# Optimization experiments

Hardware: AMD Instinct MI355X
Metric: run time of the kernel (lower is better)

Reference implementation:

```python
import jax, jax.numpy as jnp
import numpy as np

B, H, T, D = 4, 16, 2048, 128

def setup_inputs() -> dict:
    key = jax.random.key(0)
    kq, kk, kv = jax.random.split(key, 3)
    q = jax.random.normal(kq, (B, H, T, D), dtype=jnp.float32)
    k = jax.random.normal(kk, (B, H, T, D), dtype=jnp.float32)
    v = jax.random.normal(kv, (B, H, T, D), dtype=jnp.float32)
    return {"q": q, "k": k, "v": v}

def reference(q, k, v):
    # scores: [B,H,T,T] = q @ k^T, masked multiplicatively by causal lower-tri ones
    T_ = q.shape[-2]
    mask = jnp.tril(jnp.ones((T_, T_), dtype=q.dtype))  # CausalMulMask
    scores = jnp.einsum('bhid,bhjd->bhij', q, k) * mask
    # no softmax: linear attention, scores @ v
    return jnp.einsum('bhij,bhjd->bhid', scores, v)
```

## Files before the change

kernel.cpp:

```cpp
#include <hip/hip_runtime.h>
#include <stdint.h>

#define SEQ    2048
#define DIM    128
#define CHUNK  128
#define NCHUNK 16
#define NBH    64
#define DSLA   4
#define DCA    32

typedef __attribute__((ext_vector_type(8))) short short8;
typedef __attribute__((ext_vector_type(4))) float floatx4;

#define MFMA(a, b, c) __builtin_amdgcn_mfma_f32_16x16x32_bf16((a), (b), (c), 0, 0, 0)

__device__ __forceinline__ short f2bf(float f) {
  union { float f; uint32_t u; } x; x.f = f;
  uint32_t r = x.u + 0x7fffu + ((x.u >> 16) & 1u);
  return (short)(r >> 16);
}
__device__ __forceinline__ short8 pack8(const float4 a, const float4 b) {
  short8 s;
  s[0] = f2bf(a.x); s[1] = f2bf(a.y); s[2] = f2bf(a.z); s[3] = f2bf(a.w);
  s[4] = f2bf(b.x); s[5] = f2bf(b.y); s[6] = f2bf(b.z); s[7] = f2bf(b.w);
  return s;
}

__global__ __launch_bounds__(512, 2) void k_state(
    const float* __restrict__ kin, const float* __restrict__ vin,
    short* __restrict__ ws) {
  const int blk = blockIdx.x;
  const int bh  = blk & 63;
  const int dsl = blk >> 6;
  const int ds0 = dsl * DCA;
  const float* kb = kin + (size_t)bh * SEQ * DIM;
  const float* vb = vin + (size_t)bh * SEQ * DIM;

  __shared__ short Kt[128][136];
  __shared__ short Vt[DCA][136];
  __shared__ short Ss[DCA][136];

  const int tid  = threadIdx.x;
  const int wave = tid >> 6;
  const int lane = tid & 63;
  const int q4   = lane >> 4;
  const int l16  = lane & 15;
  const int j    = tid & 127;
  const int dhi  = tid >> 7;

  floatx4 acc[2];
#pragma unroll
  for (int mt = 0; mt < 2; ++mt)
#pragma unroll
    for (int r = 0; r < 4; ++r) acc[mt][r] = 0.f;

  float4 kreg[4][2], vreg[2];
  auto load_c = [&](int c) {
    const float* krow = kb + (size_t)(c * CHUNK + j) * DIM + dhi * 8;
#pragma unroll
    for (int it = 0; it < 4; ++it) {
      kreg[it][0] = *(const float4*)(krow + it * 32);
      kreg[it][1] = *(const float4*)(krow + it * 32 + 4);
    }
    const float* vrow = vb + (size_t)(c * CHUNK + j) * DIM + ds0 + dhi * 8;
    vreg[0] = *(const float4*)(vrow);
    vreg[1] = *(const float4*)(vrow + 4);
  };
  load_c(0);

  for (int c = 0; c < NCHUNK; ++c) {
    __syncthreads();

#pragma unroll
    for (int it = 0; it < 4; ++it) {
      const int d0 = it * 32 + dhi * 8;
      Kt[d0 + 0][j] = f2bf(kreg[it][0].x);
      Kt[d0 + 1][j] = f2bf(kreg[it][0].y);
      Kt[d0 + 2][j] = f2bf(kreg[it][0].z);
      Kt[d0 + 3][j] = f2bf(kreg[it][0].w);
      Kt[d0 + 4][j] = f2bf(kreg[it][1].x);
      Kt[d0 + 5][j] = f2bf(kreg[it][1].y);
      Kt[d0 + 6][j] = f2bf(kreg[it][1].z);
      Kt[d0 + 7][j] = f2bf(kreg[it][1].w);
    }
    {
      const int d0 = dhi * 8;
      Vt[d0 + 0][j] = f2bf(vreg[0].x);
      Vt[d0 + 1][j] = f2bf(vreg[0].y);
      Vt[d0 + 2][j] = f2bf(vreg[0].z);
      Vt[d0 + 3][j] = f2bf(vreg[0].w);
      Vt[d0 + 4][j] = f2bf(vreg[1].x);
      Vt[d0 + 5][j] = f2bf(vreg[1].y);
      Vt[d0 + 6][j] = f2bf(vreg[1].z);
      Vt[d0 + 7][j] = f2bf(vreg[1].w);
    }
#pragma unroll
    for (int mt = 0; mt < 2; ++mt)
#pragma unroll
      for (int r = 0; r < 4; ++r)
        Ss[mt * 16 + q4 * 4 + r][wave * 16 + l16] = f2bf(acc[mt][r]);

    __syncthreads();

    if (c + 1 < NCHUNK) load_c(c + 1);

    {
      const int ks2 = tid >> 7, tnl = (tid >> 6) & 1;
      const int q42 = (tid >> 4) & 3, l162 = tid & 15;
      const short8 sv = *(const short8*)&Ss[tnl * 16 + l162][ks2 * 32 + q42 * 8];
      *(short8*)&ws[((size_t)((bh * 16 + c) * 4 + dsl)) * 4096 + (size_t)tid * 8] = sv;
    }

#pragma unroll
    for (int ks = 0; ks < 4; ++ks) {
      const short8 bk = *(const short8*)&Kt[wave * 16 + l16][ks * 32 + q4 * 8];
#pragma unroll
      for (int mt = 0; mt < 2; ++mt) {
        const short8 av = *(const short8*)&Vt[mt * 16 + l16][ks * 32 + q4 * 8];
        acc[mt] = MFMA(av, bk, acc[mt]);
      }
    }
  }
}

__global__ __launch_bounds__(512, 2) void k_out(
    const float* __restrict__ qin, const float* __restrict__ kin,
    const float* __restrict__ vin, const short* __restrict__ ws,
    float* __restrict__ out) {
  const int blk = blockIdx.x;
  const int bh  = blk & 63;
  const int c   = blk >> 6;
  const size_t base = (size_t)bh * SEQ * DIM + (size_t)c * CHUNK * DIM;
  const float* qc = qin + base;
  const float* kc = kin + base;
  const float* vc = vin + base;
  float* oc = out + base;

  __shared__ short Klds[128][136];
  __shared__ short Vt[128][136];
  __shared__ short Ps[128][136];
  __shared__ short Sb[16384];

  const int tid  = threadIdx.x;
  const int wave = tid >> 6;
  const int lane = tid & 63;
  const int q4   = lane >> 4;
  const int l16  = lane & 15;
  const int j    = tid & 127;
  const int dhi  = tid >> 7;

  const float* qrow = qc + (size_t)(wave * 16 + l16) * DIM + q4 * 8;
  short8 aq[4];
#pragma unroll
  for (int ks = 0; ks < 4; ++ks)
    aq[ks] = pack8(*(const float4*)(qrow + ks * 32),
                   *(const float4*)(qrow + ks * 32 + 4));

#pragma unroll
  for (int it = 0; it < 4; ++it) {
    const int e = it * 4096 + tid * 8;
    *(short8*)&Klds[e >> 7][e & 127] =
        pack8(*(const float4*)(kc + e), *(const float4*)(kc + e + 4));
  }
#pragma unroll
  for (int it = 0; it < 4; ++it) {
    const int d0 = it * 32 + dhi * 8;
    const float* vrow = vc + (size_t)j * DIM + d0;
    const float4 a = *(const float4*)vrow;
    const float4 b = *(const float4*)(vrow + 4);
    Vt[d0 + 0][j] = f2bf(a.x); Vt[d0 + 1][j] = f2bf(a.y);
    Vt[d0 + 2][j] = f2bf(a.z); Vt[d0 + 3][j] = f2bf(a.w);
    Vt[d0 + 4][j] = f2bf(b.x); Vt[d0 + 5][j] = f2bf(b.y);
    Vt[d0 + 6][j] = f2bf(b.z); Vt[d0 + 7][j] = f2bf(b.w);
  }
  if (c > 0) {
    const short* sp = ws + (size_t)(bh * 16 + c) * 16384;
#pragma unroll
    for (int it = 0; it < 4; ++it) {
      const int off = it * 4096 + tid * 8;
      *(short8*)&Sb[off] = *(const short8*)&sp[off];
    }
  }
  __syncthreads();

  floatx4 oacc[8];
#pragma unroll
  for (int tn = 0; tn < 8; ++tn)
#pragma unroll
    for (int r = 0; r < 4; ++r) oacc[tn][r] = 0.f;

  if (c > 0) {
#pragma unroll
    for (int ks = 0; ks < 4; ++ks)
#pragma unroll
      for (int tn = 0; tn < 8; ++tn) {
        const short8 bs = *(const short8*)
            &Sb[(tn >> 1) * 4096 + ks * 1024 + (tn & 1) * 512 + lane * 8];
        oacc[tn] = MFMA(aq[ks], bs, oacc[tn]);
      }
  }

  for (int tj = 0; tj <= wave; ++tj) {
    floatx4 sacc;
#pragma unroll
    for (int r = 0; r < 4; ++r) sacc[r] = 0.f;
#pragma unroll
    for (int ks = 0; ks < 4; ++ks) {
      const short8 bk = *(const short8*)&Klds[tj * 16 + l16][ks * 32 + q4 * 8];
      sacc = MFMA(aq[ks], bk, sacc);
    }
#pragma unroll
    for (int r = 0; r < 4; ++r) {
      float val = sacc[r];
      if (tj == wave && l16 > q4 * 4 + r) val = 0.f;
      Ps[wave * 16 + q4 * 4 + r][tj * 16 + l16] = f2bf(val);
    }
  }
  if ((wave & 1) == 0) {
#pragma unroll
    for (int r = 0; r < 4; ++r)
      Ps[wave * 16 + q4 * 4 + r][(wave + 1) * 16 + l16] = 0;
  }

  const int kst = (wave + 2) >> 1;
  for (int t = 0; t < kst; ++t) {
    const short8 ap = *(const short8*)&Ps[wave * 16 + l16][t * 32 + q4 * 8];
#pragma unroll
    for (int tn = 0; tn < 8; ++tn) {
      const short8 bv = *(const short8*)&Vt[tn * 16 + l16][t * 32 + q4 * 8];
      oacc[tn] = MFMA(ap, bv, oacc[tn]);
    }
  }

#pragma unroll
  for (int tn = 0; tn < 8; ++tn)
#pragma unroll
    for (int r = 0; r < 4; ++r)
      oc[(size_t)(wave * 16 + q4 * 4 + r) * DIM + tn * 16 + l16] = oacc[tn][r];
}

extern "C" void kernel_launch(void* const* d_in, const int* in_sizes, int n_in,
                              void* d_out, int out_size, void* d_ws, size_t ws_size,
                              hipStream_t stream) {
  const float* q = (const float*)d_in[0];
  const float* k = (const float*)d_in[1];
  const float* v = (const float*)d_in[2];
  float* out = (float*)d_out;
  (void)in_sizes; (void)n_in; (void)out_size; (void)ws_size;
  short* ws = (short*)d_ws;

  hipLaunchKernelGGL(k_state, dim3(NBH * DSLA), dim3(512), 0, stream, k, v, ws);
  hipLaunchKernelGGL(k_out, dim3(NBH * NCHUNK), dim3(512), 0, stream,
                     q, k, v, ws, out);
}
```

Baseline: 285.0 us.

## Stage state-kernel loads via async LDS DMA and shrink output-kernel LDS

```diff
diff --git a/kernel.cpp b/kernel.cpp
--- a/kernel.cpp
+++ b/kernel.cpp
@@ -24,6 +24,11 @@
   s[0] = f2bf(a.x); s[1] = f2bf(a.y); s[2] = f2bf(a.z); s[3] = f2bf(a.w);
   s[4] = f2bf(b.x); s[5] = f2bf(b.y); s[6] = f2bf(b.z); s[7] = f2bf(b.w);
   return s;
+}
+__device__ __forceinline__ void gload16(const float* g, float* l) {
+  __builtin_amdgcn_global_load_lds(
+      (const __attribute__((address_space(1))) void*)g,
+      (__attribute__((address_space(3))) void*)l, 16, 0, 0);
 }
 
 __global__ __launch_bounds__(512, 2) void k_state(
@@ -36,6 +41,8 @@
   const float* kb = kin + (size_t)bh * SEQ * DIM;
   const float* vb = vin + (size_t)bh * SEQ * DIM;
 
+  __shared__ __align__(16) float Kf[128 * 128];
+  __shared__ __align__(16) float Vf[128 * 32];
   __shared__ short Kt[128][136];
   __shared__ short Vt[DCA][136];
   __shared__ short Ss[DCA][136];
@@ -54,45 +61,47 @@
 #pragma unroll
     for (int r = 0; r < 4; ++r) acc[mt][r] = 0.f;
 
-  float4 kreg[4][2], vreg[2];
-  auto load_c = [&](int c) {
-    const float* krow = kb + (size_t)(c * CHUNK + j) * DIM + dhi * 8;
-#pragma unroll
-    for (int it = 0; it < 4; ++it) {
-      kreg[it][0] = *(const float4*)(krow + it * 32);
-      kreg[it][1] = *(const float4*)(krow + it * 32 + 4);
-    }
-    const float* vrow = vb + (size_t)(c * CHUNK + j) * DIM + ds0 + dhi * 8;
-    vreg[0] = *(const float4*)(vrow);
-    vreg[1] = *(const float4*)(vrow + 4);
+  auto stage_async = [&](int c) {
+    const float* kc = kb + (size_t)c * CHUNK * DIM;
+#pragma unroll
+    for (int i = 0; i < 8; ++i) {
+      const int g  = i * 512 + tid;
+      const int jr = g >> 5, pq = g & 31;
+      gload16(kc + jr * DIM + ((pq ^ (jr & 7)) << 2), &Kf[g * 4]);
+    }
+    const float* vc = vb + (size_t)c * CHUNK * DIM + ds0;
+#pragma unroll
+    for (int i = 0; i < 2; ++i) {
+      const int g  = i * 512 + tid;
+      const int jr = g >> 3, pq = g & 7;
+      gload16(vc + (size_t)jr * DIM + ((pq ^ (jr & 7)) << 2), &Vf[g * 4]);
+    }
   };
-  load_c(0);
+
+  stage_async(0);
 
   for (int c = 0; c < NCHUNK; ++c) {
     __syncthreads();
 
 #pragma unroll
-    for (int it = 0; it < 4; ++it) {
-      const int d0 = it * 32 + dhi * 8;
-      Kt[d0 + 0][j] = f2bf(kreg[it][0].x);
-      Kt[d0 + 1][j] = f2bf(kreg[it][0].y);
-      Kt[d0 + 2][j] = f2bf(kreg[it][0].z);
-      Kt[d0 + 3][j] = f2bf(kreg[it][0].w);
-      Kt[d0 + 4][j] = f2bf(kreg[it][1].x);
-      Kt[d0 + 5][j] = f2bf(kreg[it][1].y);
-      Kt[d0 + 6][j] = f2bf(kreg[it][1].z);
-      Kt[d0 + 7][j] = f2bf(kreg[it][1].w);
-    }
-    {
-      const int d0 = dhi * 8;
-      Vt[d0 + 0][j] = f2bf(vreg[0].x);
-      Vt[d0 + 1][j] = f2bf(vreg[0].y);
-      Vt[d0 + 2][j] = f2bf(vreg[0].z);
-      Vt[d0 + 3][j] = f2bf(vreg[0].w);
-      Vt[d0 + 4][j] = f2bf(vreg[1].x);
-      Vt[d0 + 5][j] = f2bf(vreg[1].y);
-      Vt[d0 + 6][j] = f2bf(vreg[1].z);
-      Vt[d0 + 7][j] = f2bf(vreg[1].w);
+    for (int it = 0; it < 8; ++it) {
+      const int q = dhi * 8 + it;
+      const float4 x = *(const float4*)&Kf[(j << 7) + ((q ^ (j & 7)) << 2)];
+      const int d0 = q * 4;
+      Kt[d0 + 0][j] = f2bf(x.x);
+      Kt[d0 + 1][j] = f2bf(x.y);
+      Kt[d0 + 2][j] = f2bf(x.z);
+      Kt[d0 + 3][j] = f2bf(x.w);
+    }
+#pragma unroll
+    for (int s = 0; s < 2; ++s) {
+      const int q = dhi * 2 + s;
+      const float4 x = *(const float4*)&Vf[(j << 5) + ((q ^ (j & 7)) << 2)];
+      const int d0 = q * 4;
+      Vt[d0 + 0][j] = f2bf(x.x);
+      Vt[d0 + 1][j] = f2bf(x.y);
+      Vt[d0 + 2][j] = f2bf(x.z);
+      Vt[d0 + 3][j] = f2bf(x.w);
     }
 #pragma unroll
     for (int mt = 0; mt < 2; ++mt)
@@ -102,7 +111,7 @@
 
     __syncthreads();
 
-    if (c + 1 < NCHUNK) load_c(c + 1);
+    if (c + 1 < NCHUNK) stage_async(c + 1);
 
     {
       const int ks2 = tid >> 7, tnl = (tid >> 6) & 1;
@@ -123,7 +132,7 @@
   }
 }
 
-__global__ __launch_bounds__(512, 2) void k_out(
+__global__ __launch_bounds__(512, 4) void k_out(
     const float* __restrict__ qin, const float* __restrict__ kin,
     const float* __restrict__ vin, const short* __restrict__ ws,
     float* __restrict__ out) {
@@ -136,10 +145,8 @@
   const float* vc = vin + base;
   float* oc = out + base;
 
-  __shared__ short Klds[128][136];
+  __shared__ short KP[128][136];
   __shared__ short Vt[128][136];
-  __shared__ short Ps[128][136];
-  __shared__ short Sb[16384];
 
   const int tid  = threadIdx.x;
   const int wave = tid >> 6;
@@ -159,7 +166,7 @@
 #pragma unroll
   for (int it = 0; it < 4; ++it) {
     const int e = it * 4096 + tid * 8;
-    *(short8*)&Klds[e >> 7][e & 127] =
+    *(short8*)&KP[e >> 7][e & 127] =
         pack8(*(const float4*)(kc + e), *(const float4*)(kc + e + 4));
   }
 #pragma unroll
@@ -173,58 +180,66 @@
     Vt[d0 + 4][j] = f2bf(b.x); Vt[d0 + 5][j] = f2bf(b.y);
     Vt[d0 + 6][j] = f2bf(b.z); Vt[d0 + 7][j] = f2bf(b.w);
   }
+  __syncthreads();
+
+  floatx4 oacc[8];
+#pragma unroll
+  for (int tn = 0; tn < 8; ++tn)
+#pragma unroll
+    for (int r = 0; r < 4; ++r) oacc[tn][r] = 0.f;
+
   if (c > 0) {
     const short* sp = ws + (size_t)(bh * 16 + c) * 16384;
 #pragma unroll
-    for (int it = 0; it < 4; ++it) {
-      const int off = it * 4096 + tid * 8;
-      *(short8*)&Sb[off] = *(const short8*)&sp[off];
+    for (int ks = 0; ks < 4; ++ks)
+#pragma unroll
+      for (int tg = 0; tg < 2; ++tg) {
+        short8 bs[4];
+#pragma unroll
+        for (int t = 0; t < 4; ++t) {
+          const int tn = tg * 4 + t;
+          bs[t] = *(const short8*)
+              &sp[(tn >> 1) * 4096 + ks * 1024 + (tn & 1) * 512 + lane * 8];
+        }
+#pragma unroll
+        for (int t = 0; t < 4; ++t)
+          oacc[tg * 4 + t] = MFMA(aq[ks], bs[t], oacc[tg * 4 + t]);
+      }
+  }
+
+  floatx4 sacc[8];
+#pragma unroll
+  for (int tj = 0; tj < 8; ++tj) {
+    if (tj > wave) continue;
+#pragma unroll
+    for (int r = 0; r < 4; ++r) sacc[tj][r] = 0.f;
+#pragma unroll
+    for (int ks = 0; ks < 4; ++ks) {
+      const short8 bk = *(const short8*)&KP[tj * 16 + l16][ks * 32 + q4 * 8];
+      sacc[tj] = MFMA(aq[ks], bk, sacc[tj]);
     }
   }
   __syncthreads();
 
-  floatx4 oacc[8];
-#pragma unroll
-  for (int tn = 0; tn < 8; ++tn)
-#pragma unroll
-    for (int r = 0; r < 4; ++r) oacc[tn][r] = 0.f;
-
-  if (c > 0) {
-#pragma unroll
-    for (int ks = 0; ks < 4; ++ks)
-#pragma unroll
-      for (int tn = 0; tn < 8; ++tn) {
-        const short8 bs = *(const short8*)
-            &Sb[(tn >> 1) * 4096 + ks * 1024 + (tn & 1) * 512 + lane * 8];
-        oacc[tn] = MFMA(aq[ks], bs, oacc[tn]);
-      }
-  }
-
-  for (int tj = 0; tj <= wave; ++tj) {
-    floatx4 sacc;
-#pragma unroll
-    for (int r = 0; r < 4; ++r) sacc[r] = 0.f;
-#pragma unroll
-    for (int ks = 0; ks < 4; ++ks) {
-      const short8 bk = *(const short8*)&Klds[tj * 16 + l16][ks * 32 + q4 * 8];
-      sacc = MFMA(aq[ks], bk, sacc);
-    }
+#pragma unroll
+  for (int tj = 0; tj < 8; ++tj) {
+    if (tj > wave) continue;
 #pragma unroll
     for (int r = 0; r < 4; ++r) {
-      float val = sacc[r];
+      float val = sacc[tj][r];
       if (tj == wave && l16 > q4 * 4 + r) val = 0.f;
-      Ps[wave * 16 + q4 * 4 + r][tj * 16 + l16] = f2bf(val);
+      KP[wave * 16 + q4 * 4 + r][tj * 16 + l16] = f2bf(val);
     }
   }
   if ((wave & 1) == 0) {
 #pragma unroll
     for (int r = 0; r < 4; ++r)
-      Ps[wave * 16 + q4 * 4 + r][(wave + 1) * 16 + l16] = 0;
+      KP[wave * 16 + q4 * 4 + r][(wave + 1) * 16 + l16] = 0;
   }
 
   const int kst = (wave + 2) >> 1;
   for (int t = 0; t < kst; ++t) {
-    const short8 ap = *(const short8*)&Ps[wave * 16 + l16][t * 32 + q4 * 8];
+    const short8 ap = *(const short8*)&KP[wave * 16 + l16][t * 32 + q4 * 8];
 #pragma unroll
     for (int tn = 0; tn < 8; ++tn) {
       const short8 bv = *(const short8*)&Vt[tn * 16 + l16][t * 32 + q4 * 8];
```

New measurement: 271.1 us. -4.9%, faster.

## Replace sequential chunk-state scan with parallel per-chunk states plus prefix-sum kernel

Applied to the files above, without the earlier changes.

```diff
diff --git a/kernel.cpp b/kernel.cpp
--- a/kernel.cpp
+++ b/kernel.cpp
@@ -6,8 +6,7 @@
 #define CHUNK  128
 #define NCHUNK 16
 #define NBH    64
-#define DSLA   4
-#define DCA    32
+#define RECSH  16384
 
 typedef __attribute__((ext_vector_type(8))) short short8;
 typedef __attribute__((ext_vector_type(4))) float floatx4;
@@ -18,6 +17,11 @@
   union { float f; uint32_t u; } x; x.f = f;
   uint32_t r = x.u + 0x7fffu + ((x.u >> 16) & 1u);
   return (short)(r >> 16);
+}
+__device__ __forceinline__ float bf2f(short s) {
+  union { uint32_t u; float f; } x;
+  x.u = ((uint32_t)(uint16_t)s) << 16;
+  return x.f;
 }
 __device__ __forceinline__ short8 pack8(const float4 a, const float4 b) {
   short8 s;
@@ -25,20 +29,24 @@
   s[4] = f2bf(b.x); s[5] = f2bf(b.y); s[6] = f2bf(b.z); s[7] = f2bf(b.w);
   return s;
 }
-
-__global__ __launch_bounds__(512, 2) void k_state(
+__device__ __forceinline__ void gload16(const void* g, void* l) {
+  __builtin_amdgcn_global_load_lds(
+      (const __attribute__((address_space(1))) void*)g,
+      (__attribute__((address_space(3))) void*)l, 16, 0, 0);
+}
+
+__global__ __launch_bounds__(512, 2) void k_cstate(
     const float* __restrict__ kin, const float* __restrict__ vin,
     short* __restrict__ ws) {
   const int blk = blockIdx.x;
   const int bh  = blk & 63;
-  const int dsl = blk >> 6;
-  const int ds0 = dsl * DCA;
-  const float* kb = kin + (size_t)bh * SEQ * DIM;
-  const float* vb = vin + (size_t)bh * SEQ * DIM;
+  const int c   = blk >> 6;
+  const size_t base = (size_t)bh * SEQ * DIM + (size_t)c * CHUNK * DIM;
+  const float* kc = kin + base;
+  const float* vc = vin + base;
 
   __shared__ short Kt[128][136];
-  __shared__ short Vt[DCA][136];
-  __shared__ short Ss[DCA][136];
+  __shared__ short Vt[128][136];
 
   const int tid  = threadIdx.x;
   const int wave = tid >> 6;
@@ -48,78 +56,80 @@
   const int j    = tid & 127;
   const int dhi  = tid >> 7;
 
-  floatx4 acc[2];
-#pragma unroll
-  for (int mt = 0; mt < 2; ++mt)
-#pragma unroll
-    for (int r = 0; r < 4; ++r) acc[mt][r] = 0.f;
-
-  float4 kreg[4][2], vreg[2];
-  auto load_c = [&](int c) {
-    const float* krow = kb + (size_t)(c * CHUNK + j) * DIM + dhi * 8;
-#pragma unroll
-    for (int it = 0; it < 4; ++it) {
-      kreg[it][0] = *(const float4*)(krow + it * 32);
-      kreg[it][1] = *(const float4*)(krow + it * 32 + 4);
-    }
-    const float* vrow = vb + (size_t)(c * CHUNK + j) * DIM + ds0 + dhi * 8;
-    vreg[0] = *(const float4*)(vrow);
-    vreg[1] = *(const float4*)(vrow + 4);
-  };
-  load_c(0);
-
-  for (int c = 0; c < NCHUNK; ++c) {
-    __syncthreads();
-
-#pragma unroll
-    for (int it = 0; it < 4; ++it) {
-      const int d0 = it * 32 + dhi * 8;
-      Kt[d0 + 0][j] = f2bf(kreg[it][0].x);
-      Kt[d0 + 1][j] = f2bf(kreg[it][0].y);
-      Kt[d0 + 2][j] = f2bf(kreg[it][0].z);
-      Kt[d0 + 3][j] = f2bf(kreg[it][0].w);
-      Kt[d0 + 4][j] = f2bf(kreg[it][1].x);
-      Kt[d0 + 5][j] = f2bf(kreg[it][1].y);
-      Kt[d0 + 6][j] = f2bf(kreg[it][1].z);
-      Kt[d0 + 7][j] = f2bf(kreg[it][1].w);
-    }
-    {
-      const int d0 = dhi * 8;
-      Vt[d0 + 0][j] = f2bf(vreg[0].x);
-      Vt[d0 + 1][j] = f2bf(vreg[0].y);
-      Vt[d0 + 2][j] = f2bf(vreg[0].z);
-      Vt[d0 + 3][j] = f2bf(vreg[0].w);
-      Vt[d0 + 4][j] = f2bf(vreg[1].x);
-      Vt[d0 + 5][j] = f2bf(vreg[1].y);
-      Vt[d0 + 6][j] = f2bf(vreg[1].z);
-      Vt[d0 + 7][j] = f2bf(vreg[1].w);
-    }
-#pragma unroll
-    for (int mt = 0; mt < 2; ++mt)
-#pragma unroll
-      for (int r = 0; r < 4; ++r)
-        Ss[mt * 16 + q4 * 4 + r][wave * 16 + l16] = f2bf(acc[mt][r]);
-
-    __syncthreads();
-
-    if (c + 1 < NCHUNK) load_c(c + 1);
-
-    {
-      const int ks2 = tid >> 7, tnl = (tid >> 6) & 1;
-      const int q42 = (tid >> 4) & 3, l162 = tid & 15;
-      const short8 sv = *(const short8*)&Ss[tnl * 16 + l162][ks2 * 32 + q42 * 8];
-      *(short8*)&ws[((size_t)((bh * 16 + c) * 4 + dsl)) * 4096 + (size_t)tid * 8] = sv;
-    }
-
-#pragma unroll
-    for (int ks = 0; ks < 4; ++ks) {
-      const short8 bk = *(const short8*)&Kt[wave * 16 + l16][ks * 32 + q4 * 8];
-#pragma unroll
-      for (int mt = 0; mt < 2; ++mt) {
-        const short8 av = *(const short8*)&Vt[mt * 16 + l16][ks * 32 + q4 * 8];
-        acc[mt] = MFMA(av, bk, acc[mt]);
-      }
-    }
+#pragma unroll
+  for (int it = 0; it < 4; ++it) {
+    const int d0 = it * 32 + dhi * 8;
+    const float* krow = kc + (size_t)j * DIM + d0;
+    const float4 ka = *(const float4*)krow;
+    const float4 kb2 = *(const float4*)(krow + 4);
+    Kt[d0 + 0][j] = f2bf(ka.x); Kt[d0 + 1][j] = f2bf(ka.y);
+    Kt[d0 + 2][j] = f2bf(ka.z); Kt[d0 + 3][j] = f2bf(ka.w);
+    Kt[d0 + 4][j] = f2bf(kb2.x); Kt[d0 + 5][j] = f2bf(kb2.y);
+    Kt[d0 + 6][j] = f2bf(kb2.z); Kt[d0 + 7][j] = f2bf(kb2.w);
+    const float* vrow = vc + (size_t)j * DIM + d0;
+    const float4 va = *(const float4*)vrow;
+    const float4 vb2 = *(const float4*)(vrow + 4);
+    Vt[d0 + 0][j] = f2bf(va.x); Vt[d0 + 1][j] = f2bf(va.y);
+    Vt[d0 + 2][j] = f2bf(va.z); Vt[d0 + 3][j] = f2bf(va.w);
+    Vt[d0 + 4][j] = f2bf(vb2.x); Vt[d0 + 5][j] = f2bf(vb2.y);
+    Vt[d0 + 6][j] = f2bf(vb2.z); Vt[d0 + 7][j] = f2bf(vb2.w);
+  }
+  __syncthreads();
+
+  floatx4 acc[8];
+#pragma unroll
+  for (int m = 0; m < 8; ++m)
+#pragma unroll
+    for (int r = 0; r < 4; ++r) acc[m][r] = 0.f;
+#pragma unroll
+  for (int ks = 0; ks < 4; ++ks) {
+    const short8 bk = *(const short8*)&Kt[wave * 16 + l16][ks * 32 + q4 * 8];
+#pragma unroll
+    for (int m = 0; m < 8; ++m) {
+      const short8 av = *(const short8*)&Vt[m * 16 + l16][ks * 32 + q4 * 8];
+      acc[m] = MFMA(av, bk, acc[m]);
+    }
+  }
+  __syncthreads();
+
+  short (*Ss)[136] = (short (*)[136])Kt;
+#pragma unroll
+  for (int m = 0; m < 8; ++m)
+#pragma unroll
+    for (int r = 0; r < 4; ++r)
+      Ss[m * 16 + q4 * 4 + r][wave * 16 + l16] = f2bf(acc[m][r]);
+  __syncthreads();
+
+  short* rec = ws + (size_t)(bh * NCHUNK + c) * RECSH;
+#pragma unroll
+  for (int i = 0; i < 4; ++i) {
+    const int t8  = i * 512 + tid;
+    const int row = ((t8 >> 9) << 5) + (((t8 >> 6) & 1) << 4) + (t8 & 15);
+    const int col = (((t8 >> 7) & 3) << 5) + (((t8 >> 4) & 3) << 3);
+    *(short8*)&rec[(size_t)t8 * 8] = *(const short8*)&Ss[row][col];
+  }
+}
+
+__global__ __launch_bounds__(256, 4) void k_prefix(short* __restrict__ ws) {
+  const int blk = blockIdx.x;
+  const int bh  = blk & 63;
+  const int p   = blk >> 6;
+  const int off = p * 2048 + threadIdx.x * 8;
+  short* wb = ws + (size_t)bh * NCHUNK * RECSH;
+
+  float run[8];
+#pragma unroll
+  for (int s = 0; s < 8; ++s) run[s] = 0.f;
+#pragma unroll
+  for (int cc = 0; cc < NCHUNK; ++cc) {
+    short8* ptr = (short8*)&wb[(size_t)cc * RECSH + off];
+    const short8 rv = *ptr;
+    short8 ov;
+#pragma unroll
+    for (int s = 0; s < 8; ++s) ov[s] = f2bf(run[s]);
+    *ptr = ov;
+#pragma unroll
+    for (int s = 0; s < 8; ++s) run[s] += bf2f(rv[s]);
   }
 }
 
@@ -139,7 +149,7 @@
   __shared__ short Klds[128][136];
   __shared__ short Vt[128][136];
   __shared__ short Ps[128][136];
-  __shared__ short Sb[16384];
+  __shared__ __align__(16) short Sb[RECSH];
 
   const int tid  = threadIdx.x;
   const int wave = tid >> 6;
@@ -148,6 +158,13 @@
   const int l16  = lane & 15;
   const int j    = tid & 127;
   const int dhi  = tid >> 7;
+
+  const short* sp = ws + (size_t)(bh * NCHUNK + c) * RECSH;
+#pragma unroll
+  for (int i = 0; i < 4; ++i) {
+    const int g = i * 512 + tid;
+    gload16(&sp[(size_t)g * 8], &Sb[(size_t)g * 8]);
+  }
 
   const float* qrow = qc + (size_t)(wave * 16 + l16) * DIM + q4 * 8;
   short8 aq[4];
@@ -173,14 +190,6 @@
     Vt[d0 + 4][j] = f2bf(b.x); Vt[d0 + 5][j] = f2bf(b.y);
     Vt[d0 + 6][j] = f2bf(b.z); Vt[d0 + 7][j] = f2bf(b.w);
   }
-  if (c > 0) {
-    const short* sp = ws + (size_t)(bh * 16 + c) * 16384;
-#pragma unroll
-    for (int it = 0; it < 4; ++it) {
-      const int off = it * 4096 + tid * 8;
-      *(short8*)&Sb[off] = *(const short8*)&sp[off];
-    }
-  }
   __syncthreads();
 
   floatx4 oacc[8];
@@ -189,16 +198,14 @@
 #pragma unroll
     for (int r = 0; r < 4; ++r) oacc[tn][r] = 0.f;
 
-  if (c > 0) {
-#pragma unroll
-    for (int ks = 0; ks < 4; ++ks)
-#pragma unroll
-      for (int tn = 0; tn < 8; ++tn) {
-        const short8 bs = *(const short8*)
-            &Sb[(tn >> 1) * 4096 + ks * 1024 + (tn & 1) * 512 + lane * 8];
-        oacc[tn] = MFMA(aq[ks], bs, oacc[tn]);
-      }
-  }
+#pragma unroll
+  for (int ks = 0; ks < 4; ++ks)
+#pragma unroll
+    for (int tn = 0; tn < 8; ++tn) {
+      const short8 bs = *(const short8*)
+          &Sb[(tn >> 1) * 4096 + ks * 1024 + (tn & 1) * 512 + lane * 8];
+      oacc[tn] = MFMA(aq[ks], bs, oacc[tn]);
+    }
 
   for (int tj = 0; tj <= wave; ++tj) {
     floatx4 sacc;
@@ -249,7 +256,9 @@
   (void)in_sizes; (void)n_in; (void)out_size; (void)ws_size;
   short* ws = (short*)d_ws;
 
-  hipLaunchKernelGGL(k_state, dim3(NBH * DSLA), dim3(512), 0, stream, k, v, ws);
+  hipLaunchKernelGGL(k_cstate, dim3(NBH * NCHUNK), dim3(512), 0, stream,
+                     k, v, ws);
+  hipLaunchKernelGGL(k_prefix, dim3(NBH * 8), dim3(256), 0, stream, ws);
   hipLaunchKernelGGL(k_out, dim3(NBH * NCHUNK), dim3(512), 0, stream,
                      q, k, v, ws, out);
 }
```

Result: faster. 275.9 us (-3.2%).
